# Kernel tuning notes

Measured on AMD Instinct MI355X. Metric: run time of the kernel, lower is better.

## Reference

```python
import jax, jax.numpy as jnp
import numpy as np

B = 131072      # flattened batch of item embeddings
E = 256         # e_dim; x has 2*E features (src half, rec half)
NQ = 4          # residual quantizer levels per branch
NE = 256        # codebook size per level
BETA = 0.25


def setup_inputs() -> dict:
    key = jax.random.key(0)
    k1, k2, k3 = jax.random.split(key, 3)
    x = jax.random.normal(k1, (B, 2 * E), dtype=jnp.float32)
    src_codebooks = jax.random.normal(k2, (NQ, NE, E), dtype=jnp.float32)
    rec_codebooks = jax.random.normal(k3, (NQ, NE, E), dtype=jnp.float32)
    return {"x": x, "src_codebooks": src_codebooks, "rec_codebooks": rec_codebooks}


def _vq(residual, cb):
    # residual: [B, E], cb: [NE, E]
    # squared euclidean distances via expanded form (GEMM-dominated)
    d = (jnp.sum(residual * residual, axis=1, keepdims=True)
         - 2.0 * (residual @ cb.T)
         + jnp.sum(cb * cb, axis=1)[None, :])          # [B, NE]
    idx = jnp.argmin(d, axis=1)                          # [B]
    x_q = cb[idx]                                        # gather [B, E]
    loss = (jnp.mean((jax.lax.stop_gradient(x_q) - residual) ** 2)
            + BETA * jnp.mean((x_q - jax.lax.stop_gradient(residual)) ** 2))
    # straight-through estimator
    x_q = residual + jax.lax.stop_gradient(x_q - residual)
    return x_q, loss, idx


def _rq(x_part, codebooks):
    # sequential residual VQ chain over NQ levels (small fixed unroll)
    residual = x_part
    x_q = jnp.zeros_like(x_part)
    losses, indices = [], []
    for i in range(codebooks.shape[0]):
        x_res, l, idx = _vq(residual, codebooks[i])
        residual = residual - x_res
        x_q = x_q + x_res
        losses.append(l)
        indices.append(idx)
    return x_q, jnp.stack(losses), jnp.stack(indices, axis=-1)


def reference(x, src_codebooks, rec_codebooks):
    src_x_q, src_l, src_idx = _rq(x[:, :E], src_codebooks)
    rec_x_q, rec_l, rec_idx = _rq(x[:, E:], rec_codebooks)
    mean_loss = jnp.mean(jnp.concatenate([src_l, rec_l]))
    return ((src_x_q, rec_x_q), mean_loss, (src_idx, rec_idx))
```

## Files before the change

### kernel.cpp

```cpp
#include <hip/hip_runtime.h>
#include <hip/hip_bf16.h>
#include <hip/hip_fp16.h>
#include <cstdint>
#include <cstddef>

#define NB   131072
#define ED   256
#define NQL  4
#define NEC  256

typedef _Float16 f16;
typedef f16  f16x8 __attribute__((ext_vector_type(8)));
typedef float f32x4 __attribute__((ext_vector_type(4)));

static constexpr float FMAXV = 3.402823466e+38f;
static constexpr float TAUH  = 0.078125f;

static constexpr size_t OFF_REC  = (size_t)NB * ED;
static constexpr size_t OFF_LOSS = 2 * (size_t)NB * ED;
static constexpr size_t OFF_SIDX = OFF_LOSS + 1;
static constexpr size_t OFF_RIDX = OFF_SIDX + (size_t)NB * NQL;

static constexpr size_t WS_LOSS = 0;
static constexpr size_t WS_NORM = 256;
static constexpr size_t WS_CBH  = 256 + 8 * 256 * 4;

__global__ void kPrep(const float* __restrict__ cbS, const float* __restrict__ cbR,
                      float* __restrict__ norms, double* __restrict__ lossAcc) {
  const int cbi = blockIdx.x;
  const int j   = threadIdx.x;
  if (cbi == 0 && j < 8) lossAcc[j] = 0.0;
  const float* row = (cbi < 4 ? cbS : cbR) + ((size_t)(cbi & 3) * NEC + j) * ED;
  float acc = 0.f;
  for (int k = 0; k < ED; k += 4) {
    float4 v = *(const float4*)(row + k);
    acc += v.x * v.x + v.y * v.y + v.z * v.z + v.w * v.w;
  }
  norms[cbi * NEC + j] = acc - 256.0f;
}

__global__ void kConvH(const float* __restrict__ cbS, const float* __restrict__ cbR,
                       f16* __restrict__ cbH) {
  const int f   = blockIdx.x * 256 + threadIdx.x;
  const int cbi = f >> 16;
  const int rem = f & 65535;
  const float v = (cbi < 4 ? cbS + ((size_t)cbi << 16) : cbR + ((size_t)(cbi - 4) << 16))[rem];
  cbH[f] = (f16)(-v);
}

__device__ __forceinline__ float pk(float v, int j) {
  return __uint_as_float((__float_as_uint(v) & ~255u) | (unsigned)j);
}
__device__ __forceinline__ float unpv(float k) {
  return __uint_as_float(__float_as_uint(k) & ~255u);
}
__device__ __forceinline__ void ins3(float& s0, float& s1, float& s2, float k) {
  float t0 = fmaxf(s0, k); s0 = fminf(s0, k);
  float t1 = fmaxf(s1, t0); s1 = fminf(s1, t0);
  s2 = fminf(s2, t1);
}
__device__ __forceinline__ void mrg3(float& a0, float& a1, float& a2,
                                     float b0, float b1, float b2) {
  float x  = fmaxf(a0, b0);
  float c0 = fminf(a0, b0);
  float m1 = fminf(a1, b1), M1 = fmaxf(a1, b1);
  float c1 = fminf(fminf(x, a1), b1);
  float c2 = fminf(fminf(fmaxf(x, m1), M1), fminf(a2, b2));
  a0 = c0; a1 = c1; a2 = c2;
}

__global__ __launch_bounds__(256, 2)
void kMain(const float* __restrict__ x,
           const float* __restrict__ cbS,
           const float* __restrict__ cbR,
           const f16*  __restrict__ cbH,
           const float* __restrict__ norms,
           double* __restrict__ lossAcc,
           float* __restrict__ out) {
  __shared__ __align__(16) char  RhBuf[64 * 512];
  __shared__ __align__(16) float keybuf[64][4][4];
  __shared__ float redS[4];

  const int tid   = threadIdx.x;
  const int lane  = tid & 63;
  const int w     = tid >> 6;
  const int it_o  = tid >> 2;
  const int kq    = tid & 3;
  const int b0    = blockIdx.x * 64;
  const int br    = blockIdx.y;
  const int l15   = lane & 15;
  const int l4    = lane >> 4;

  const float* cbf32base = br ? cbR : cbS;
  float res[64];
  float lossA = 0.f, lossB = 0.f;

  {
    const float* xp = x + (size_t)(b0 + it_o) * (2 * ED) + br * ED + kq * 64;
#pragma unroll
    for (int i = 0; i < 16; ++i) {
      float4 v = *(const float4*)(xp + 4 * i);
      res[4 * i + 0] = v.x; res[4 * i + 1] = v.y;
      res[4 * i + 2] = v.z; res[4 * i + 3] = v.w;
    }
  }

#pragma unroll 1
  for (int lev = 0; lev < NQL; ++lev) {
    const int cbi = br * 4 + lev;
    const float* nrm = norms + (size_t)cbi * NEC;
    const f16*   cbh = cbH + ((size_t)cbi << 16);
    const float* cbf32 = cbf32base + (size_t)lev * NEC * ED;

#pragma unroll
    for (int c = 0; c < 8; ++c) {
      f16x8 h;
#pragma unroll
      for (int u = 0; u < 8; ++u) h[u] = (f16)res[c * 8 + u];
      int off = it_o * 512 + kq * 128 + c * 16;
      off ^= (it_o & 7) << 4;
      *(f16x8*)&RhBuf[off] = h;
    }
    __syncthreads();

    f32x4 acc[4][4];
#pragma unroll
    for (int nt = 0; nt < 4; ++nt) {
      float4 nv = *(const float4*)&nrm[w * 64 + nt * 16 + l4 * 4];
      f32x4 h; h[0] = 0.5f * nv.x; h[1] = 0.5f * nv.y;
      h[2] = 0.5f * nv.z; h[3] = 0.5f * nv.w;
#pragma unroll
      for (int mt = 0; mt < 4; ++mt) acc[mt][nt] = h;
    }

    f16x8 A0[4], B0[4], A1[4], B1[4];
#define LOADA(Adst, ks_)                                                        \
    {                                                                           \
      _Pragma("unroll")                                                         \
      for (int mt = 0; mt < 4; ++mt) {                                          \
        const int it = mt * 16 + l15;                                           \
        const int offA = (it * 512 + (ks_) * 64 + l4 * 16) ^ ((it & 7) << 4);   \
        Adst[mt] = *(const f16x8*)&RhBuf[offA];                                 \
      }                                                                         \
    }
#define LOADB(Bdst, ks_)                                                        \
    {                                                                           \
      _Pragma("unroll")                                                         \
      for (int nt = 0; nt < 4; ++nt) {                                          \
        const int j = w * 64 + nt * 16 + l15;                                   \
        Bdst[nt] = *(const f16x8*)&cbh[(size_t)j * ED + (ks_) * 32 + l4 * 8];   \
      }                                                                         \
    }
#define MFMA16(Aop, Bop)                                                        \
    {                                                                           \
      __builtin_amdgcn_s_setprio(1);                                            \
      _Pragma("unroll")                                                         \
      for (int mt = 0; mt < 4; ++mt)                                            \
        _Pragma("unroll")                                                       \
        for (int nt = 0; nt < 4; ++nt)                                          \
          acc[mt][nt] = __builtin_amdgcn_mfma_f32_16x16x32_f16(                 \
              Bop[nt], Aop[mt], acc[mt][nt], 0, 0, 0);                          \
      __builtin_amdgcn_s_setprio(0);                                            \
    }

    LOADA(A0, 0); LOADB(B0, 0);
#pragma unroll 1
    for (int ks2 = 0; ks2 < 4; ++ks2) {
      LOADA(A1, 2 * ks2 + 1); LOADB(B1, 2 * ks2 + 1);
      MFMA16(A0, B0);
      if (ks2 < 3) { LOADA(A0, 2 * ks2 + 2); LOADB(B0, 2 * ks2 + 2); }
      MFMA16(A1, B1);
    }
#undef LOADA
#undef LOADB
#undef MFMA16

#pragma unroll
    for (int mt = 0; mt < 4; ++mt) {
      float s0 = FMAXV, s1 = FMAXV, s2 = FMAXV;
#pragma unroll
      for (int nt = 0; nt < 4; ++nt)
#pragma unroll
        for (int r = 0; r < 4; ++r)
          ins3(s0, s1, s2, pk(acc[mt][nt][r], w * 64 + nt * 16 + l4 * 4 + r));
      {
        float b0k = __shfl_xor(s0, 16), b1k = __shfl_xor(s1, 16), b2k = __shfl_xor(s2, 16);
        mrg3(s0, s1, s2, b0k, b1k, b2k);
        b0k = __shfl_xor(s0, 32); b1k = __shfl_xor(s1, 32); b2k = __shfl_xor(s2, 32);
        mrg3(s0, s1, s2, b0k, b1k, b2k);
      }
      if (l4 == 0) {
        float4 v; v.x = s0; v.y = s1; v.z = s2; v.w = FMAXV;
        *(float4*)&keybuf[mt * 16 + l15][w][0] = v;
      }
    }
    __syncthreads();

    int jm;
    {
      float4 v = *(const float4*)&keybuf[it_o][kq][0];
      float s0 = v.x, s1 = v.y, s2 = v.z;
      {
        float b0k = __shfl_xor(s0, 1), b1k = __shfl_xor(s1, 1), b2k = __shfl_xor(s2, 1);
        mrg3(s0, s1, s2, b0k, b1k, b2k);
        b0k = __shfl_xor(s0, 2); b1k = __shfl_xor(s1, 2); b2k = __shfl_xor(s2, 2);
        mrg3(s0, s1, s2, b0k, b1k, b2k);
      }
      jm = (int)(__float_as_uint(s0) & 255u);
      const float gap = unpv(s1) - unpv(s0);
      if (gap < TAUH) {
        const int cand[3] = { jm, (int)(__float_as_uint(s1) & 255u),
                                  (int)(__float_as_uint(s2) & 255u) };
        float bestd = FMAXV; int bestj = 0;
#pragma unroll 1
        for (int cc = 0; cc < 3; ++cc) {
          const int j = cand[cc];
          const float* row = cbf32 + (size_t)j * ED + kq * 64;
          float p2 = 0.f;
#pragma unroll
          for (int i = 0; i < 16; ++i) {
            float4 q = *(const float4*)(row + 4 * i);
            p2 = fmaf(res[4 * i + 0], q.x, p2);
            p2 = fmaf(res[4 * i + 1], q.y, p2);
            p2 = fmaf(res[4 * i + 2], q.z, p2);
            p2 = fmaf(res[4 * i + 3], q.w, p2);
          }
          p2 += __shfl_xor(p2, 1);
          p2 += __shfl_xor(p2, 2);
          const float d = fmaf(-2.f, p2, nrm[j]);
          if (d < bestd || (d == bestd && j < bestj)) { bestd = d; bestj = j; }
        }
        jm = bestj;
      }
      if (kq == 0) {
        const size_t ioff = (br ? OFF_RIDX : OFF_SIDX) + (size_t)(b0 + it_o) * NQL + lev;
        out[ioff] = (float)jm;
      }
    }

    {
      const float* crow = cbf32 + (size_t)jm * ED + kq * 64;
#pragma unroll
      for (int i = 0; i < 16; ++i) {
        float4 q = *(const float4*)(crow + 4 * i);
#pragma unroll
        for (int u = 0; u < 4; ++u) {
          float cv = (u == 0 ? q.x : u == 1 ? q.y : u == 2 ? q.z : q.w);
          float r  = res[4 * i + u];
          float dd = cv - r;
          if (u & 1) lossB = fmaf(dd, dd, lossB);
          else       lossA = fmaf(dd, dd, lossA);
          float xr = r + dd;
          res[4 * i + u] = r - xr;
        }
      }
    }
  }

  {
    const float* xp = x + (size_t)(b0 + it_o) * (2 * ED) + br * ED + kq * 64;
    float* op = out + (br ? OFF_REC : 0) + (size_t)(b0 + it_o) * ED + kq * 64;
#pragma unroll
    for (int i = 0; i < 16; ++i) {
      float4 xv = *(const float4*)(xp + 4 * i);
      float4 o;
      o.x = xv.x - res[4 * i + 0];
      o.y = xv.y - res[4 * i + 1];
      o.z = xv.z - res[4 * i + 2];
      o.w = xv.w - res[4 * i + 3];
      *(float4*)(op + 4 * i) = o;
    }
  }

  float lossReg = lossA + lossB;
#pragma unroll
  for (int d = 1; d < 64; d <<= 1) lossReg += __shfl_xor(lossReg, d);
  if (lane == 0) redS[w] = lossReg;
  __syncthreads();
  if (tid == 0)
    atomicAdd(&lossAcc[blockIdx.x & 7], (double)((redS[0] + redS[1]) + (redS[2] + redS[3])));
}

__global__ void kFin(const double* __restrict__ lossAcc, float* __restrict__ out) {
  if (blockIdx.x == 0 && threadIdx.x == 0) {
    double s = 0.0;
    for (int l = 0; l < 8; ++l) s += lossAcc[l];
    out[OFF_LOSS] = (float)(s * 1.25 / ((double)NB * ED) / 8.0);
  }
}

extern "C" void kernel_launch(void* const* d_in, const int* in_sizes, int n_in,
                              void* d_out, int out_size, void* d_ws, size_t ws_size,
                              hipStream_t stream) {
  const float* x   = (const float*)d_in[0];
  const float* cbS = (const float*)d_in[1];
  const float* cbR = (const float*)d_in[2];
  float* out = (float*)d_out;
  char*  ws  = (char*)d_ws;

  double* lossAcc = (double*)(ws + WS_LOSS);
  float*  norms   = (float*)(ws + WS_NORM);
  f16*    cbH     = (f16*)(ws + WS_CBH);

  hipLaunchKernelGGL(kPrep,  dim3(8),    dim3(256), 0, stream, cbS, cbR, norms, lossAcc);
  hipLaunchKernelGGL(kConvH, dim3(2048), dim3(256), 0, stream, cbS, cbR, cbH);
  hipLaunchKernelGGL(kMain,  dim3(NB / 64, 2), dim3(256), 0, stream,
                     x, cbS, cbR, cbH, norms, lossAcc, out);
  hipLaunchKernelGGL(kFin,   dim3(1),    dim3(64),  0, stream, lossAcc, out);
}
```

Baseline: 558.4 us.

## Process both src and rec branches per block for 32 items

Each block now handles 32 items across both branches (src rows in the first half, rec rows in the second) instead of 64 items of one branch. The GEMM loads both codebooks' B fragments and applies them to their matching A tiles. The explicit double-buffered register prefetch is replaced by a simple unroll-2 loop. The likely goal is more even work per block and better locality on x rows, since both halves of each x row are read by the same block. The cost is twice the B-fragment global loads per MFMA and the loss of the hand-written software pipelining.

```diff
diff --git a/kernel.cpp b/kernel.cpp
--- a/kernel.cpp
+++ b/kernel.cpp
@@ -86,17 +86,18 @@
   const int w     = tid >> 6;
   const int it_o  = tid >> 2;
   const int kq    = tid & 3;
-  const int b0    = blockIdx.x * 64;
-  const int br    = blockIdx.y;
+  const int vbr   = it_o >> 5;
+  const int item  = it_o & 31;
+  const int b0    = blockIdx.x * 32;
   const int l15   = lane & 15;
   const int l4    = lane >> 4;
 
-  const float* cbf32base = br ? cbR : cbS;
+  const float* cbf32base = vbr ? cbR : cbS;
   float res[64];
   float lossA = 0.f, lossB = 0.f;
 
   {
-    const float* xp = x + (size_t)(b0 + it_o) * (2 * ED) + br * ED + kq * 64;
+    const float* xp = x + (size_t)(b0 + item) * (2 * ED) + vbr * ED + kq * 64;
 #pragma unroll
     for (int i = 0; i < 16; ++i) {
       float4 v = *(const float4*)(xp + 4 * i);
@@ -107,9 +108,11 @@
 
 #pragma unroll 1
   for (int lev = 0; lev < NQL; ++lev) {
-    const int cbi = br * 4 + lev;
-    const float* nrm = norms + (size_t)cbi * NEC;
-    const f16*   cbh = cbH + ((size_t)cbi << 16);
+    const float* nrmS = norms + (size_t)lev * NEC;
+    const float* nrmR = norms + (size_t)(4 + lev) * NEC;
+    const f16*   cbhS = cbH + ((size_t)lev << 16);
+    const f16*   cbhR = cbH + ((size_t)(4 + lev) << 16);
+    const float* nrmO  = vbr ? nrmR : nrmS;
     const float* cbf32 = cbf32base + (size_t)lev * NEC * ED;
 
 #pragma unroll
@@ -126,54 +129,39 @@
     f32x4 acc[4][4];
 #pragma unroll
     for (int nt = 0; nt < 4; ++nt) {
-      float4 nv = *(const float4*)&nrm[w * 64 + nt * 16 + l4 * 4];
-      f32x4 h; h[0] = 0.5f * nv.x; h[1] = 0.5f * nv.y;
-      h[2] = 0.5f * nv.z; h[3] = 0.5f * nv.w;
-#pragma unroll
-      for (int mt = 0; mt < 4; ++mt) acc[mt][nt] = h;
-    }
-
-    f16x8 A0[4], B0[4], A1[4], B1[4];
-#define LOADA(Adst, ks_)                                                        \
-    {                                                                           \
-      _Pragma("unroll")                                                         \
-      for (int mt = 0; mt < 4; ++mt) {                                          \
-        const int it = mt * 16 + l15;                                           \
-        const int offA = (it * 512 + (ks_) * 64 + l4 * 16) ^ ((it & 7) << 4);   \
-        Adst[mt] = *(const f16x8*)&RhBuf[offA];                                 \
-      }                                                                         \
-    }
-#define LOADB(Bdst, ks_)                                                        \
-    {                                                                           \
-      _Pragma("unroll")                                                         \
-      for (int nt = 0; nt < 4; ++nt) {                                          \
-        const int j = w * 64 + nt * 16 + l15;                                   \
-        Bdst[nt] = *(const f16x8*)&cbh[(size_t)j * ED + (ks_) * 32 + l4 * 8];   \
-      }                                                                         \
-    }
-#define MFMA16(Aop, Bop)                                                        \
-    {                                                                           \
-      __builtin_amdgcn_s_setprio(1);                                            \
-      _Pragma("unroll")                                                         \
-      for (int mt = 0; mt < 4; ++mt)                                            \
-        _Pragma("unroll")                                                       \
-        for (int nt = 0; nt < 4; ++nt)                                          \
-          acc[mt][nt] = __builtin_amdgcn_mfma_f32_16x16x32_f16(                 \
-              Bop[nt], Aop[mt], acc[mt][nt], 0, 0, 0);                          \
-      __builtin_amdgcn_s_setprio(0);                                            \
-    }
-
-    LOADA(A0, 0); LOADB(B0, 0);
-#pragma unroll 1
-    for (int ks2 = 0; ks2 < 4; ++ks2) {
-      LOADA(A1, 2 * ks2 + 1); LOADB(B1, 2 * ks2 + 1);
-      MFMA16(A0, B0);
-      if (ks2 < 3) { LOADA(A0, 2 * ks2 + 2); LOADB(B0, 2 * ks2 + 2); }
-      MFMA16(A1, B1);
-    }
-#undef LOADA
-#undef LOADB
-#undef MFMA16
+      float4 nS = *(const float4*)&nrmS[w * 64 + nt * 16 + l4 * 4];
+      float4 nR = *(const float4*)&nrmR[w * 64 + nt * 16 + l4 * 4];
+      f32x4 hS; hS[0] = 0.5f * nS.x; hS[1] = 0.5f * nS.y; hS[2] = 0.5f * nS.z; hS[3] = 0.5f * nS.w;
+      f32x4 hR; hR[0] = 0.5f * nR.x; hR[1] = 0.5f * nR.y; hR[2] = 0.5f * nR.z; hR[3] = 0.5f * nR.w;
+      acc[0][nt] = hS; acc[1][nt] = hS;
+      acc[2][nt] = hR; acc[3][nt] = hR;
+    }
+
+#pragma unroll 2
+    for (int ks = 0; ks < 8; ++ks) {
+      f16x8 A[4], Bs[4], Br[4];
+#pragma unroll
+      for (int mt = 0; mt < 4; ++mt) {
+        const int it = mt * 16 + l15;
+        const int offA = (it * 512 + ks * 64 + l4 * 16) ^ ((it & 7) << 4);
+        A[mt] = *(const f16x8*)&RhBuf[offA];
+      }
+#pragma unroll
+      for (int nt = 0; nt < 4; ++nt) {
+        const int j = w * 64 + nt * 16 + l15;
+        Bs[nt] = *(const f16x8*)&cbhS[(size_t)j * ED + ks * 32 + l4 * 8];
+        Br[nt] = *(const f16x8*)&cbhR[(size_t)j * ED + ks * 32 + l4 * 8];
+      }
+      __builtin_amdgcn_s_setprio(1);
+#pragma unroll
+      for (int nt = 0; nt < 4; ++nt) {
+        acc[0][nt] = __builtin_amdgcn_mfma_f32_16x16x32_f16(Bs[nt], A[0], acc[0][nt], 0, 0, 0);
+        acc[1][nt] = __builtin_amdgcn_mfma_f32_16x16x32_f16(Bs[nt], A[1], acc[1][nt], 0, 0, 0);
+        acc[2][nt] = __builtin_amdgcn_mfma_f32_16x16x32_f16(Br[nt], A[2], acc[2][nt], 0, 0, 0);
+        acc[3][nt] = __builtin_amdgcn_mfma_f32_16x16x32_f16(Br[nt], A[3], acc[3][nt], 0, 0, 0);
+      }
+      __builtin_amdgcn_s_setprio(0);
+    }
 
 #pragma unroll
     for (int mt = 0; mt < 4; ++mt) {
@@ -227,13 +215,13 @@
           }
           p2 += __shfl_xor(p2, 1);
           p2 += __shfl_xor(p2, 2);
-          const float d = fmaf(-2.f, p2, nrm[j]);
+          const float d = fmaf(-2.f, p2, nrmO[j]);
           if (d < bestd || (d == bestd && j < bestj)) { bestd = d; bestj = j; }
         }
         jm = bestj;
       }
       if (kq == 0) {
-        const size_t ioff = (br ? OFF_RIDX : OFF_SIDX) + (size_t)(b0 + it_o) * NQL + lev;
+        const size_t ioff = (vbr ? OFF_RIDX : OFF_SIDX) + (size_t)(b0 + item) * NQL + lev;
         out[ioff] = (float)jm;
       }
     }
@@ -258,8 +246,8 @@
   }
 
   {
-    const float* xp = x + (size_t)(b0 + it_o) * (2 * ED) + br * ED + kq * 64;
-    float* op = out + (br ? OFF_REC : 0) + (size_t)(b0 + it_o) * ED + kq * 64;
+    const float* xp = x + (size_t)(b0 + item) * (2 * ED) + vbr * ED + kq * 64;
+    float* op = out + (vbr ? OFF_REC : 0) + (size_t)(b0 + item) * ED + kq * 64;
 #pragma unroll
     for (int i = 0; i < 16; ++i) {
       float4 xv = *(const float4*)(xp + 4 * i);
@@ -304,7 +292,7 @@
 
   hipLaunchKernelGGL(kPrep,  dim3(8),    dim3(256), 0, stream, cbS, cbR, norms, lossAcc);
   hipLaunchKernelGGL(kConvH, dim3(2048), dim3(256), 0, stream, cbS, cbR, cbH);
-  hipLaunchKernelGGL(kMain,  dim3(NB / 64, 2), dim3(256), 0, stream,
+  hipLaunchKernelGGL(kMain,  dim3(NB / 32), dim3(256), 0, stream,
                      x, cbS, cbR, cbH, norms, lossAcc, out);
   hipLaunchKernelGGL(kFin,   dim3(1),    dim3(64),  0, stream, lossAcc, out);
 }
```

Result: slower. 753.3 us (+34.9%).
